# Optimization experiments

Hardware: AMD Instinct MI355X
Metric: run time of the kernel (lower is better)

## Reference

```python
import jax, jax.numpy as jnp
import numpy as np
from jax import lax

NPOINT = 1024
NSAMPLE = 32
RADIUS = 0.2
EPS = 1e-5  # BatchNorm eps


def _fps(xyz, npoint):
    """Farthest point sampling (deterministic, start at index 0). xyz: (B,N,3) -> idx (B,npoint)."""
    B, N, _ = xyz.shape
    big = jnp.asarray(1e10, xyz.dtype)

    def step(carry, _):
        min_d, last = carry
        cent = xyz[jnp.arange(B), last]                      # (B,3)
        d = jnp.sum((xyz - cent[:, None, :]) ** 2, axis=-1)  # (B,N)
        min_d = jnp.minimum(min_d, d)
        nxt = jnp.argmax(min_d, axis=-1).astype(jnp.int32)
        return (min_d, nxt), last

    init = (jnp.full((B, N), big, xyz.dtype), jnp.zeros((B,), jnp.int32))
    _, idxs = lax.scan(step, init, None, length=npoint)      # (npoint,B)
    return idxs.T                                            # (B,npoint)


def _ball_query(new_xyz, xyz, K, radius):
    """First-K-within-radius neighbors (pytorch3d semantics: pad idx=-1, nn=0)."""
    B, S, _ = new_xyz.shape
    N = xyz.shape[1]
    d2 = jnp.sum((new_xyz[:, :, None, :] - xyz[:, None, :, :]) ** 2, axis=-1)  # (B,S,N)
    mask = d2 < radius * radius
    key = jnp.where(mask, jnp.arange(N, dtype=jnp.int32), jnp.int32(N))
    idx = jnp.sort(key, axis=-1)[..., :K]                    # (B,S,K) first K hits in order
    valid = idx < N
    idx = jnp.where(valid, idx, -1)
    idx_safe = jnp.where(valid, idx, 0)
    g = jnp.take_along_axis(xyz, idx_safe.reshape(B, S * K)[:, :, None], axis=1)
    grouped_xyz = jnp.where(valid[..., None], g.reshape(B, S, K, 3), 0.0)      # padded -> 0
    return idx, grouped_xyz


def _gather_points(points, idx):
    """index_points with torch negative-index semantics (-1 wraps to N-1)."""
    B, N, D = points.shape
    S, K = idx.shape[1], idx.shape[2]
    idx_w = jnp.where(idx < 0, idx + N, idx)
    g = jnp.take_along_axis(points, idx_w.reshape(B, S * K)[:, :, None], axis=1)
    return g.reshape(B, S, K, D)


def _forward(xyz, points, params):
    B, N, C = xyz.shape
    fps_idx = _fps(xyz, NPOINT)                                          # (B,S)
    new_xyz = jnp.take_along_axis(xyz, fps_idx[:, :, None], axis=1)      # (B,S,3)
    idx, grouped_xyz = _ball_query(new_xyz, xyz, NSAMPLE, RADIUS)        # (B,S,K),(B,S,K,3)
    grouped_xyz_norm = grouped_xyz - new_xyz[:, :, None, :]
    grouped_points = _gather_points(points, idx)                         # (B,S,K,D)
    x = jnp.concatenate([grouped_xyz_norm, grouped_points], axis=-1)     # (B,S,K,3+D)
    for (W, b, g, be, m, v) in params:
        x = jnp.einsum('bskc,cd->bskd', x, W) + b                        # 1x1 conv over channels
        x = (x - m) * (g * lax.rsqrt(v + EPS)) + be                      # BN (eval mode)
        x = jax.nn.relu(x)
    new_points = jnp.max(x, axis=2)                                      # max over neighbors -> (B,S,C')
    return new_xyz, new_points


def setup_inputs() -> dict:
    key = jax.random.key(0)
    ks = jax.random.split(key, 32)
    B, N, D = 16, 4096, 64
    mlp = [64, 64, 128]
    inp = {
        'xyz': jax.random.uniform(ks[0], (B, N, 3), jnp.float32),
        'points': jax.random.normal(ks[1], (B, N, D), jnp.float32),
    }
    cin = 3 + D
    k = 2
    for i, cout in enumerate(mlp):
        inp[f'W{i}'] = jax.random.normal(ks[k], (cin, cout), jnp.float32) * (1.0 / np.sqrt(cin)); k += 1
        inp[f'b{i}'] = jax.random.normal(ks[k], (cout,), jnp.float32) * 0.01; k += 1
        inp[f'g{i}'] = jax.random.uniform(ks[k], (cout,), jnp.float32) + 0.5; k += 1
        inp[f'be{i}'] = jax.random.normal(ks[k], (cout,), jnp.float32) * 0.01; k += 1
        inp[f'm{i}'] = jax.random.normal(ks[k], (cout,), jnp.float32) * 0.01; k += 1
        inp[f'v{i}'] = jax.random.uniform(ks[k], (cout,), jnp.float32) + 0.5; k += 1
        cin = cout
    return inp


def reference(xyz, points, W0, b0, g0, be0, m0, v0,
              W1, b1, g1, be1, m1, v1,
              W2, b2, g2, be2, m2, v2):
    params = [(W0, b0, g0, be0, m0, v0),
              (W1, b1, g1, be1, m1, v1),
              (W2, b2, g2, be2, m2, v2)]
    return _forward(xyz, points, params)
```

## Files before the change

kernel.cpp:

```cpp
#include <hip/hip_runtime.h>


typedef unsigned int   u32;
typedef unsigned long long u64;

#define NB 16
#define NP 4096
#define NS 1024
#define NK 32
#define NITEM (NB * NS / 2)

#define DPP_UPD(v, ctrl) ((u32)__builtin_amdgcn_update_dpp((int)(v), (int)(v), (ctrl), 0xf, 0xf, false))
#define U64_STEP(v, ctrl) { \
  u32 _lo = DPP_UPD((u32)(v), ctrl); \
  u32 _hi = DPP_UPD((u32)((v) >> 32), ctrl); \
  u64 _o = (((u64)_hi) << 32) | _lo; \
  v = (v > _o) ? v : _o; }
#define WAVE_RED_U64MAX(v) do { U64_STEP(v,0x111); U64_STEP(v,0x112); U64_STEP(v,0x114); \
                                U64_STEP(v,0x118); U64_STEP(v,0x142); U64_STEP(v,0x143); } while (0)
#define UMAX_DPP(v, ctrl) { u32 _o = DPP_UPD(v, ctrl); v = (v > _o) ? v : _o; }
#define HALF_RED_UMAX32(v) do { UMAX_DPP(v,0x111); UMAX_DPP(v,0x112); UMAX_DPP(v,0x114); \
                                UMAX_DPP(v,0x118); UMAX_DPP(v,0x142); } while (0)

struct FpsS { float4 pt[NP]; u64 red[2][4]; };
struct HalfS {
  float x0[64 * 67];
  u64 masks[2][64];
  int offs[2][64];
  int idx_ls[2][NK];
  float cent[8];
};
struct ConS { HalfS h[2]; float sAB[512]; int shi; };
union SMem { FpsS f; ConS c; };

__device__ __forceinline__ float dload_f(const float* p) {
  return __uint_as_float(__hip_atomic_load((const u32*)p, __ATOMIC_RELAXED, __HIP_MEMORY_SCOPE_AGENT));
}

__global__ void __launch_bounds__(512)
fused_kernel(const float* __restrict__ xyz, const float* __restrict__ pts,
             const float* __restrict__ W0, const float* __restrict__ b0, const float* __restrict__ g0,
             const float* __restrict__ be0, const float* __restrict__ m0, const float* __restrict__ v0,
             const float* __restrict__ W1, const float* __restrict__ b1, const float* __restrict__ g1,
             const float* __restrict__ be1, const float* __restrict__ m1, const float* __restrict__ v1,
             const float* __restrict__ W2, const float* __restrict__ b2, const float* __restrict__ g2,
             const float* __restrict__ be2, const float* __restrict__ m2, const float* __restrict__ v2,
             float* __restrict__ out0, float* __restrict__ out1,
             int* __restrict__ progress, int* __restrict__ ctr)
{
  __shared__ SMem sm;
  const int t = threadIdx.x;

  if (blockIdx.x < NB) {
    asm volatile("s_setprio 3");
    FpsS& S = sm.f;
    const int b = blockIdx.x;
    const int lane = t & 63, wv = t >> 6;
    const float* bx = xyz + (size_t)b * NP * 3;
    for (int i = t; i < NP; i += 512) {
      S.pt[i] = make_float4(bx[i * 3 + 0], bx[i * 3 + 1], bx[i * 3 + 2], 0.0f);
    }
    __syncthreads();

    if (wv < 4) {
      float px[16], py[16], pz[16], md[16];
#pragma unroll
      for (int p = 0; p < 16; ++p) {
        float4 f4 = S.pt[p * 256 + t];
        px[p] = f4.x; py[p] = f4.y; pz[p] = f4.z;
        md[p] = 1e10f;
      }
      const u32 nt = ~(u32)t;
      float4 c4 = S.pt[0];
      float cx = c4.x, cy = c4.y, cz = c4.z;
      float hx = cx, hy = cy, hz = cz;

      for (int it = 1; it < NS; ++it) {
        u32 vb, ca;
        {
          float dx = __fsub_rn(px[0], cx);
          float dy = __fsub_rn(py[0], cy);
          float dz = __fsub_rn(pz[0], cz);
          float d  = __fadd_rn(__fadd_rn(__fmul_rn(dx, dx), __fmul_rn(dy, dy)), __fmul_rn(dz, dz));
          float m2 = fminf(md[0], d);
          md[0] = m2;
          vb = __float_as_uint(m2);
          ca = nt;
        }
#pragma unroll
        for (int p = 1; p < 16; ++p) {
          float dx = __fsub_rn(px[p], cx);
          float dy = __fsub_rn(py[p], cy);
          float dz = __fsub_rn(pz[p], cz);
          float d  = __fadd_rn(__fadd_rn(__fmul_rn(dx, dx), __fmul_rn(dy, dy)), __fmul_rn(dz, dz));
          float m2 = fminf(md[p], d);
          md[p] = m2;
          u32 mb = __float_as_uint(m2);
          bool gt = mb > vb;
          vb = gt ? mb : vb;
          ca = gt ? (nt - (u32)(p * 256)) : ca;
        }
        u64 key = (((u64)vb) << 32) | ca;
        WAVE_RED_U64MAX(key);
        const int par = it & 1;
        if (lane == 63) S.red[par][wv] = key;
        __syncthreads();
        u64 k0 = S.red[par][0], k1 = S.red[par][1], k2 = S.red[par][2], k3 = S.red[par][3];
        u64 m01 = (k0 > k1) ? k0 : k1;
        u64 m23 = (k2 > k3) ? k2 : k3;
        u64 bk = (m01 > m23) ? m01 : m23;
        const int idx = (int)(~(u32)bk);
        float4 cc = S.pt[idx];
        cx = cc.x; cy = cc.y; cz = cc.z;
        if (wv == 0) {
          bool cap = (lane == (it & 15));
          hx = cap ? cx : hx;
          hy = cap ? cy : hy;
          hz = cap ? cz : hz;
          if ((it & 15) == 15) {
            if (lane < 16) {
              float* o = out0 + ((size_t)b * NS + (it - 15) + lane) * 3;
              o[0] = hx; o[1] = hy; o[2] = hz;
            }
            if (lane == 0)
              __hip_atomic_store(&progress[b * 16], it + 1, __ATOMIC_RELEASE, __HIP_MEMORY_SCOPE_AGENT);
          }
        }
      }
    } else {
      for (int it = 1; it < NS; ++it) __syncthreads();
    }
    return;
  }

  ConS& C = sm.c;
  const int half = t >> 8;
  const int u = t & 255;
  const int lane = t & 63;
  const int hw = u >> 6;
  HalfS& H = C.h[half];
  const float R2 = (float)(0.2 * 0.2);

  if (t < 256) {
    const float *gp, *bep, *mp, *vp, *bpp; int c, base, bcoff;
    if (t < 64)       { c = t;       gp = g0; bep = be0; mp = m0; vp = v0; bpp = b0; base = 0;   bcoff = 64;  }
    else if (t < 128) { c = t - 64;  gp = g1; bep = be1; mp = m1; vp = v1; bpp = b1; base = 128; bcoff = 64;  }
    else              { c = t - 128; gp = g2; bep = be2; mp = m2; vp = v2; bpp = b2; base = 256; bcoff = 128; }
    float a = gp[c] / sqrtf(vp[c] + 1e-5f);
    C.sAB[base + c] = a;
    C.sAB[base + bcoff + c] = (bpp[c] - mp[c]) * a + bep[c];
  }
  __syncthreads();

  for (;;) {
    if (t == 0) C.shi = atomicAdd(ctr, 2);
    __syncthreads();
    const int i0 = C.shi;
    if (i0 >= NITEM) break;
    const int item = i0 + half;
    const bool active = item < NITEM;
    const int b = item & 15, pr = item >> 4, s0 = pr * 2;

    if (u == 0 && active) {
      const int need = s0 + 2;
      while (__hip_atomic_load(&progress[b * 16], __ATOMIC_ACQUIRE, __HIP_MEMORY_SCOPE_AGENT) < need)
        __builtin_amdgcn_s_sleep(32);
      const float* cp = out0 + ((size_t)b * NS + s0) * 3;
#pragma unroll
      for (int i2 = 0; i2 < 6; ++i2) H.cent[i2] = dload_f(cp + i2);
    }
    __syncthreads();
    const float c0x = H.cent[0], c0y = H.cent[1], c0z = H.cent[2];
    const float c1x = H.cent[3], c1y = H.cent[4], c1z = H.cent[5];
    const float* bx = xyz + (size_t)b * NP * 3;

    if (active) {
      for (int c = 0; c < 16; ++c) {
        int ch = hw * 16 + c;
        int i = ch * 64 + lane;
        float X = bx[i * 3 + 0], Y = bx[i * 3 + 1], Z = bx[i * 3 + 2];
        float dx0 = __fsub_rn(c0x, X), dy0 = __fsub_rn(c0y, Y), dz0 = __fsub_rn(c0z, Z);
        float d20 = __fadd_rn(__fadd_rn(__fmul_rn(dx0, dx0), __fmul_rn(dy0, dy0)), __fmul_rn(dz0, dz0));
        u64 mA = __ballot(d20 < R2);
        float dx1 = __fsub_rn(c1x, X), dy1 = __fsub_rn(c1y, Y), dz1 = __fsub_rn(c1z, Z);
        float d21 = __fadd_rn(__fadd_rn(__fmul_rn(dx1, dx1), __fmul_rn(dy1, dy1)), __fmul_rn(dz1, dz1));
        u64 mB = __ballot(d21 < R2);
        if (lane == 0) { H.masks[0][ch] = mA; H.masks[1][ch] = mB; }
      }
      if (u < 64) H.idx_ls[u >> 5][u & 31] = -1;
    }
    __syncthreads();
    if (active && (hw & 1) == 0) {
      int cent = hw >> 1;
      int cnt = __popcll(H.masks[cent][lane]);
      int inc = cnt;
#pragma unroll
      for (int off = 1; off < 64; off <<= 1) {
        int n = __shfl_up(inc, off);
        if (lane >= off) inc += n;
      }
      H.offs[cent][lane] = inc - cnt;
    }
    __syncthreads();
    if (active) {
      for (int c = 0; c < 16; ++c) {
        int ch = hw * 16 + c;
#pragma unroll
        for (int cent = 0; cent < 2; ++cent) {
          int base = H.offs[cent][ch];
          if (base >= NK) continue;
          u64 m = H.masks[cent][ch];
          if ((m >> lane) & 1ull) {
            int slot = base + __popcll(m & ((1ull << lane) - 1ull));
            if (slot < NK) H.idx_ls[cent][slot] = ch * 64 + lane;
          }
        }
      }
    }
    __syncthreads();
    if (active) {
      int cent = u >> 7, tt = u & 127;
      int row = tt >> 2, q = tt & 3;
      int id = H.idx_ls[cent][row];
      int prow = (id < 0) ? (NP - 1) : id;
      const float4* p4 = (const float4*)(pts + ((size_t)b * NP + prow) * 64 + q * 16);
      float4 va = p4[0], vb = p4[1], vc = p4[2], vd = p4[3];
      float* dst = &H.x0[(cent * 32 + row) * 67 + 3 + q * 16];
      dst[0]  = va.x; dst[1]  = va.y; dst[2]  = va.z; dst[3]  = va.w;
      dst[4]  = vb.x; dst[5]  = vb.y; dst[6]  = vb.z; dst[7]  = vb.w;
      dst[8]  = vc.x; dst[9]  = vc.y; dst[10] = vc.z; dst[11] = vc.w;
      dst[12] = vd.x; dst[13] = vd.y; dst[14] = vd.z; dst[15] = vd.w;
      if (u < 64) {
        int c2 = u >> 5, slot = u & 31;
        int id2 = H.idx_ls[c2][slot];
        float ax = c2 ? c1x : c0x, ay = c2 ? c1y : c0y, az = c2 ? c1z : c0z;
        float gx, gy, gz;
        if (id2 >= 0) {
          gx = __fsub_rn(bx[id2 * 3 + 0], ax);
          gy = __fsub_rn(bx[id2 * 3 + 1], ay);
          gz = __fsub_rn(bx[id2 * 3 + 2], az);
        } else {
          gx = 0.0f - ax; gy = 0.0f - ay; gz = 0.0f - az;
        }
        float* d2p = &H.x0[(c2 * 32 + slot) * 67];
        d2p[0] = gx; d2p[1] = gy; d2p[2] = gz;
      }
    }
    __syncthreads();

    const int j0 = __builtin_amdgcn_readfirstlane(hw * 16);
    {
      float acc[16];
#pragma unroll
      for (int i = 0; i < 16; ++i) acc[i] = 0.0f;
      if (active) {
        const float* xr = &H.x0[lane * 67];
#pragma unroll 2
        for (int c = 0; c < 67; ++c) {
          float xv = xr[c];
          const float4* wr = (const float4*)(W0 + c * 64 + j0);
          float4 wa = wr[0], wb = wr[1], wc = wr[2], wd = wr[3];
          acc[0]  = fmaf(xv, wa.x, acc[0]);  acc[1]  = fmaf(xv, wa.y, acc[1]);
          acc[2]  = fmaf(xv, wa.z, acc[2]);  acc[3]  = fmaf(xv, wa.w, acc[3]);
          acc[4]  = fmaf(xv, wb.x, acc[4]);  acc[5]  = fmaf(xv, wb.y, acc[5]);
          acc[6]  = fmaf(xv, wb.z, acc[6]);  acc[7]  = fmaf(xv, wb.w, acc[7]);
          acc[8]  = fmaf(xv, wc.x, acc[8]);  acc[9]  = fmaf(xv, wc.y, acc[9]);
          acc[10] = fmaf(xv, wc.z, acc[10]); acc[11] = fmaf(xv, wc.w, acc[11]);
          acc[12] = fmaf(xv, wd.x, acc[12]); acc[13] = fmaf(xv, wd.y, acc[13]);
          acc[14] = fmaf(xv, wd.z, acc[14]); acc[15] = fmaf(xv, wd.w, acc[15]);
        }
      }
      __syncthreads();
      if (active) {
#pragma unroll
        for (int i = 0; i < 16; ++i) {
          float y = fmaf(acc[i], C.sAB[j0 + i], C.sAB[64 + j0 + i]);
          H.x0[lane * 67 + j0 + i] = fmaxf(y, 0.0f);
        }
      }
    }
    __syncthreads();
    {
      float acc[16];
#pragma unroll
      for (int i = 0; i < 16; ++i) acc[i] = 0.0f;
      if (active) {
        const float* xr = &H.x0[lane * 67];
#pragma unroll 2
        for (int c = 0; c < 64; ++c) {
          float xv = xr[c];
          const float4* wr = (const float4*)(W1 + c * 64 + j0);
          float4 wa = wr[0], wb = wr[1], wc = wr[2], wd = wr[3];
          acc[0]  = fmaf(xv, wa.x, acc[0]);  acc[1]  = fmaf(xv, wa.y, acc[1]);
          acc[2]  = fmaf(xv, wa.z, acc[2]);  acc[3]  = fmaf(xv, wa.w, acc[3]);
          acc[4]  = fmaf(xv, wb.x, acc[4]);  acc[5]  = fmaf(xv, wb.y, acc[5]);
          acc[6]  = fmaf(xv, wb.z, acc[6]);  acc[7]  = fmaf(xv, wb.w, acc[7]);
          acc[8]  = fmaf(xv, wc.x, acc[8]);  acc[9]  = fmaf(xv, wc.y, acc[9]);
          acc[10] = fmaf(xv, wc.z, acc[10]); acc[11] = fmaf(xv, wc.w, acc[11]);
          acc[12] = fmaf(xv, wd.x, acc[12]); acc[13] = fmaf(xv, wd.y, acc[13]);
          acc[14] = fmaf(xv, wd.z, acc[14]); acc[15] = fmaf(xv, wd.w, acc[15]);
        }
      }
      __syncthreads();
      if (active) {
#pragma unroll
        for (int i = 0; i < 16; ++i) {
          float y = fmaf(acc[i], C.sAB[128 + j0 + i], C.sAB[192 + j0 + i]);
          H.x0[lane * 67 + j0 + i] = fmaxf(y, 0.0f);
        }
      }
    }
    __syncthreads();
    if (active) {
      const int j3 = __builtin_amdgcn_readfirstlane(hw * 32);
      float acc[32];
#pragma unroll
      for (int i = 0; i < 32; ++i) acc[i] = 0.0f;
      const float* xr = &H.x0[lane * 67];
      for (int c = 0; c < 64; ++c) {
        float xv = xr[c];
        const float4* wr = (const float4*)(W2 + c * 128 + j3);
#pragma unroll
        for (int q = 0; q < 8; ++q) {
          float4 wq = wr[q];
          acc[q * 4 + 0] = fmaf(xv, wq.x, acc[q * 4 + 0]);
          acc[q * 4 + 1] = fmaf(xv, wq.y, acc[q * 4 + 1]);
          acc[q * 4 + 2] = fmaf(xv, wq.z, acc[q * 4 + 2]);
          acc[q * 4 + 3] = fmaf(xv, wq.w, acc[q * 4 + 3]);
        }
      }
#pragma unroll
      for (int i = 0; i < 32; ++i) {
        float y = fmaf(acc[i], C.sAB[256 + j3 + i], C.sAB[384 + j3 + i]);
        u32 mb = __float_as_uint(fmaxf(y, 0.0f));
        HALF_RED_UMAX32(mb);
        acc[i] = __uint_as_float(mb);
      }
      if (lane == 31 || lane == 63) {
        int cent = lane >> 5;
        float4* op = (float4*)(out1 + ((size_t)b * NS + s0 + cent) * 128 + j3);
#pragma unroll
        for (int q = 0; q < 8; ++q)
          op[q] = make_float4(acc[q * 4 + 0], acc[q * 4 + 1], acc[q * 4 + 2], acc[q * 4 + 3]);
      }
    }
  }
}

extern "C" void kernel_launch(void* const* d_in, const int* in_sizes, int n_in,
                              void* d_out, int out_size, void* d_ws, size_t ws_size,
                              hipStream_t stream) {
  const float* xyz = (const float*)d_in[0];
  const float* pts = (const float*)d_in[1];
  const float* W0 = (const float*)d_in[2];  const float* b0 = (const float*)d_in[3];
  const float* g0 = (const float*)d_in[4];  const float* be0 = (const float*)d_in[5];
  const float* m0 = (const float*)d_in[6];  const float* v0 = (const float*)d_in[7];
  const float* W1 = (const float*)d_in[8];  const float* b1 = (const float*)d_in[9];
  const float* g1 = (const float*)d_in[10]; const float* be1 = (const float*)d_in[11];
  const float* m1 = (const float*)d_in[12]; const float* v1 = (const float*)d_in[13];
  const float* W2 = (const float*)d_in[14]; const float* b2 = (const float*)d_in[15];
  const float* g2 = (const float*)d_in[16]; const float* be2 = (const float*)d_in[17];
  const float* m2 = (const float*)d_in[18]; const float* v2 = (const float*)d_in[19];

  float* out0 = (float*)d_out;
  float* out1 = out0 + NB * NS * 3;
  int* prog = (int*)d_ws;
  int* ctr  = (int*)d_ws + 320;

  hipMemsetAsync(d_ws, 0, 2048, stream);

  fused_kernel<<<256, 512, 0, stream>>>(
      xyz, pts,
      W0, b0, g0, be0, m0, v0,
      W1, b1, g1, be1, m1, v1,
      W2, b2, g2, be2, m2, v2,
      out0, out1, prog, ctr);
}
```

Baseline: 766.7 us.

## Shrink blocks to 256 threads, one work item per consumer block

Blocks go from 512 threads to 256. The FPS producer blocks no longer carry four idle waves that only spin on barriers, and each consumer block now processes a single item instead of two halves sharing one block. The aim is to cut barrier overhead and idle waves and to let more independent blocks run per CU, which also loosens the register limit. The grid is still 256 blocks, so the consumer blocks now have half the threads, and throughput depends on whether occupancy rises enough to compensate.

```diff
diff --git a/kernel.cpp b/kernel.cpp
--- a/kernel.cpp
+++ b/kernel.cpp
@@ -30,14 +30,14 @@
   int idx_ls[2][NK];
   float cent[8];
 };
-struct ConS { HalfS h[2]; float sAB[512]; int shi; };
+struct ConS { HalfS h; float sAB[512]; int shi; };
 union SMem { FpsS f; ConS c; };
 
 __device__ __forceinline__ float dload_f(const float* p) {
   return __uint_as_float(__hip_atomic_load((const u32*)p, __ATOMIC_RELAXED, __HIP_MEMORY_SCOPE_AGENT));
 }
 
-__global__ void __launch_bounds__(512)
+__global__ void __launch_bounds__(256)
 fused_kernel(const float* __restrict__ xyz, const float* __restrict__ pts,
              const float* __restrict__ W0, const float* __restrict__ b0, const float* __restrict__ g0,
              const float* __restrict__ be0, const float* __restrict__ m0, const float* __restrict__ v0,
@@ -57,91 +57,86 @@
     const int b = blockIdx.x;
     const int lane = t & 63, wv = t >> 6;
     const float* bx = xyz + (size_t)b * NP * 3;
-    for (int i = t; i < NP; i += 512) {
+    for (int i = t; i < NP; i += 256) {
       S.pt[i] = make_float4(bx[i * 3 + 0], bx[i * 3 + 1], bx[i * 3 + 2], 0.0f);
     }
     __syncthreads();
 
-    if (wv < 4) {
-      float px[16], py[16], pz[16], md[16];
-#pragma unroll
-      for (int p = 0; p < 16; ++p) {
-        float4 f4 = S.pt[p * 256 + t];
-        px[p] = f4.x; py[p] = f4.y; pz[p] = f4.z;
-        md[p] = 1e10f;
-      }
-      const u32 nt = ~(u32)t;
-      float4 c4 = S.pt[0];
-      float cx = c4.x, cy = c4.y, cz = c4.z;
-      float hx = cx, hy = cy, hz = cz;
-
-      for (int it = 1; it < NS; ++it) {
-        u32 vb, ca;
-        {
-          float dx = __fsub_rn(px[0], cx);
-          float dy = __fsub_rn(py[0], cy);
-          float dz = __fsub_rn(pz[0], cz);
-          float d  = __fadd_rn(__fadd_rn(__fmul_rn(dx, dx), __fmul_rn(dy, dy)), __fmul_rn(dz, dz));
-          float m2 = fminf(md[0], d);
-          md[0] = m2;
-          vb = __float_as_uint(m2);
-          ca = nt;
-        }
-#pragma unroll
-        for (int p = 1; p < 16; ++p) {
-          float dx = __fsub_rn(px[p], cx);
-          float dy = __fsub_rn(py[p], cy);
-          float dz = __fsub_rn(pz[p], cz);
-          float d  = __fadd_rn(__fadd_rn(__fmul_rn(dx, dx), __fmul_rn(dy, dy)), __fmul_rn(dz, dz));
-          float m2 = fminf(md[p], d);
-          md[p] = m2;
-          u32 mb = __float_as_uint(m2);
-          bool gt = mb > vb;
-          vb = gt ? mb : vb;
-          ca = gt ? (nt - (u32)(p * 256)) : ca;
-        }
-        u64 key = (((u64)vb) << 32) | ca;
-        WAVE_RED_U64MAX(key);
-        const int par = it & 1;
-        if (lane == 63) S.red[par][wv] = key;
-        __syncthreads();
-        u64 k0 = S.red[par][0], k1 = S.red[par][1], k2 = S.red[par][2], k3 = S.red[par][3];
-        u64 m01 = (k0 > k1) ? k0 : k1;
-        u64 m23 = (k2 > k3) ? k2 : k3;
-        u64 bk = (m01 > m23) ? m01 : m23;
-        const int idx = (int)(~(u32)bk);
-        float4 cc = S.pt[idx];
-        cx = cc.x; cy = cc.y; cz = cc.z;
-        if (wv == 0) {
-          bool cap = (lane == (it & 15));
-          hx = cap ? cx : hx;
-          hy = cap ? cy : hy;
-          hz = cap ? cz : hz;
-          if ((it & 15) == 15) {
-            if (lane < 16) {
-              float* o = out0 + ((size_t)b * NS + (it - 15) + lane) * 3;
-              o[0] = hx; o[1] = hy; o[2] = hz;
-            }
-            if (lane == 0)
-              __hip_atomic_store(&progress[b * 16], it + 1, __ATOMIC_RELEASE, __HIP_MEMORY_SCOPE_AGENT);
+    float px[16], py[16], pz[16], md[16];
+#pragma unroll
+    for (int p = 0; p < 16; ++p) {
+      float4 f4 = S.pt[p * 256 + t];
+      px[p] = f4.x; py[p] = f4.y; pz[p] = f4.z;
+      md[p] = 1e10f;
+    }
+    const u32 nt = ~(u32)t;
+    float4 c4 = S.pt[0];
+    float cx = c4.x, cy = c4.y, cz = c4.z;
+    float hx = cx, hy = cy, hz = cz;
+
+    for (int it = 1; it < NS; ++it) {
+      u32 vb, ca;
+      {
+        float dx = __fsub_rn(px[0], cx);
+        float dy = __fsub_rn(py[0], cy);
+        float dz = __fsub_rn(pz[0], cz);
+        float d  = __fadd_rn(__fadd_rn(__fmul_rn(dx, dx), __fmul_rn(dy, dy)), __fmul_rn(dz, dz));
+        float m2 = fminf(md[0], d);
+        md[0] = m2;
+        vb = __float_as_uint(m2);
+        ca = nt;
+      }
+#pragma unroll
+      for (int p = 1; p < 16; ++p) {
+        float dx = __fsub_rn(px[p], cx);
+        float dy = __fsub_rn(py[p], cy);
+        float dz = __fsub_rn(pz[p], cz);
+        float d  = __fadd_rn(__fadd_rn(__fmul_rn(dx, dx), __fmul_rn(dy, dy)), __fmul_rn(dz, dz));
+        float m2 = fminf(md[p], d);
+        md[p] = m2;
+        u32 mb = __float_as_uint(m2);
+        bool gt = mb > vb;
+        vb = gt ? mb : vb;
+        ca = gt ? (nt - (u32)(p * 256)) : ca;
+      }
+      u64 key = (((u64)vb) << 32) | ca;
+      WAVE_RED_U64MAX(key);
+      const int par = it & 1;
+      if (lane == 63) S.red[par][wv] = key;
+      __syncthreads();
+      u64 k0 = S.red[par][0], k1 = S.red[par][1], k2 = S.red[par][2], k3 = S.red[par][3];
+      u64 m01 = (k0 > k1) ? k0 : k1;
+      u64 m23 = (k2 > k3) ? k2 : k3;
+      u64 bk = (m01 > m23) ? m01 : m23;
+      const int idx = (int)(~(u32)bk);
+      float4 cc = S.pt[idx];
+      cx = cc.x; cy = cc.y; cz = cc.z;
+      if (wv == 0) {
+        bool cap = (lane == (it & 15));
+        hx = cap ? cx : hx;
+        hy = cap ? cy : hy;
+        hz = cap ? cz : hz;
+        if ((it & 15) == 15) {
+          if (lane < 16) {
+            float* o = out0 + ((size_t)b * NS + (it - 15) + lane) * 3;
+            o[0] = hx; o[1] = hy; o[2] = hz;
           }
-        }
-      }
-    } else {
-      for (int it = 1; it < NS; ++it) __syncthreads();
+          if (lane == 0)
+            __hip_atomic_store(&progress[b * 16], it + 1, __ATOMIC_RELEASE, __HIP_MEMORY_SCOPE_AGENT);
+        }
+      }
     }
     return;
   }
 
   ConS& C = sm.c;
-  const int half = t >> 8;
-  const int u = t & 255;
+  const int u = t;
   const int lane = t & 63;
   const int hw = u >> 6;
-  HalfS& H = C.h[half];
+  HalfS& H = C.h;
   const float R2 = (float)(0.2 * 0.2);
 
-  if (t < 256) {
+  {
     const float *gp, *bep, *mp, *vp, *bpp; int c, base, bcoff;
     if (t < 64)       { c = t;       gp = g0; bep = be0; mp = m0; vp = v0; bpp = b0; base = 0;   bcoff = 64;  }
     else if (t < 128) { c = t - 64;  gp = g1; bep = be1; mp = m1; vp = v1; bpp = b1; base = 128; bcoff = 64;  }
@@ -153,15 +148,13 @@
   __syncthreads();
 
   for (;;) {
-    if (t == 0) C.shi = atomicAdd(ctr, 2);
-    __syncthreads();
-    const int i0 = C.shi;
-    if (i0 >= NITEM) break;
-    const int item = i0 + half;
-    const bool active = item < NITEM;
+    if (t == 0) C.shi = atomicAdd(ctr, 1);
+    __syncthreads();
+    const int item = C.shi;
+    if (item >= NITEM) break;
     const int b = item & 15, pr = item >> 4, s0 = pr * 2;
 
-    if (u == 0 && active) {
+    if (u == 0) {
       const int need = s0 + 2;
       while (__hip_atomic_load(&progress[b * 16], __ATOMIC_ACQUIRE, __HIP_MEMORY_SCOPE_AGENT) < need)
         __builtin_amdgcn_s_sleep(32);
@@ -174,7 +167,7 @@
     const float c1x = H.cent[3], c1y = H.cent[4], c1z = H.cent[5];
     const float* bx = xyz + (size_t)b * NP * 3;
 
-    if (active) {
+    {
       for (int c = 0; c < 16; ++c) {
         int ch = hw * 16 + c;
         int i = ch * 64 + lane;
@@ -190,7 +183,7 @@
       if (u < 64) H.idx_ls[u >> 5][u & 31] = -1;
     }
     __syncthreads();
-    if (active && (hw & 1) == 0) {
+    if ((hw & 1) == 0) {
       int cent = hw >> 1;
       int cnt = __popcll(H.masks[cent][lane]);
       int inc = cnt;
@@ -202,7 +195,7 @@
       H.offs[cent][lane] = inc - cnt;
     }
     __syncthreads();
-    if (active) {
+    {
       for (int c = 0; c < 16; ++c) {
         int ch = hw * 16 + c;
 #pragma unroll
@@ -218,7 +211,7 @@
       }
     }
     __syncthreads();
-    if (active) {
+    {
       int cent = u >> 7, tt = u & 127;
       int row = tt >> 2, q = tt & 3;
       int id = H.idx_ls[cent][row];
@@ -253,7 +246,7 @@
       float acc[16];
 #pragma unroll
       for (int i = 0; i < 16; ++i) acc[i] = 0.0f;
-      if (active) {
+      {
         const float* xr = &H.x0[lane * 67];
 #pragma unroll 2
         for (int c = 0; c < 67; ++c) {
@@ -271,7 +264,7 @@
         }
       }
       __syncthreads();
-      if (active) {
+      {
 #pragma unroll
         for (int i = 0; i < 16; ++i) {
           float y = fmaf(acc[i], C.sAB[j0 + i], C.sAB[64 + j0 + i]);
@@ -284,7 +277,7 @@
       float acc[16];
 #pragma unroll
       for (int i = 0; i < 16; ++i) acc[i] = 0.0f;
-      if (active) {
+      {
         const float* xr = &H.x0[lane * 67];
 #pragma unroll 2
         for (int c = 0; c < 64; ++c) {
@@ -302,7 +295,7 @@
         }
       }
       __syncthreads();
-      if (active) {
+      {
 #pragma unroll
         for (int i = 0; i < 16; ++i) {
           float y = fmaf(acc[i], C.sAB[128 + j0 + i], C.sAB[192 + j0 + i]);
@@ -311,7 +304,7 @@
       }
     }
     __syncthreads();
-    if (active) {
+    {
       const int j3 = __builtin_amdgcn_readfirstlane(hw * 32);
       float acc[32];
 #pragma unroll
@@ -369,7 +362,7 @@
 
   hipMemsetAsync(d_ws, 0, 2048, stream);
 
-  fused_kernel<<<256, 512, 0, stream>>>(
+  fused_kernel<<<256, 256, 0, stream>>>(
       xyz, pts,
       W0, b0, g0, be0, m0, v0,
       W1, b1, g1, be1, m1, v1,
```

After: 1.104 ms. 1.44x slower.
